# Kernel tuning notes

Hardware: AMD Instinct MI355X
Metric: run time of the kernel (lower is better)

Reference implementation:

```python
import jax, jax.numpy as jnp
import numpy as np

N, E = 50000, 400000
DIN, DH, H, DOUT = 128, 32, 10, 32
HID = H * DH
NEG = 0.2          # LeakyReLU slope in GATv2
EPS_BN = 1e-5

def setup_inputs():
    key = jax.random.key(0)
    ks = jax.random.split(key, 10)
    g = lambda k, shape, fan: jax.random.normal(k, shape, jnp.float32) * (1.0 / np.sqrt(fan))
    return {
        "x": jax.random.normal(ks[0], (N, DIN), jnp.float32),
        "edge_index": jax.random.randint(ks[1], (2, E), 0, N),
        "Wl1": g(ks[2], (DIN, HID), DIN), "bl1": jnp.zeros((HID,), jnp.float32),
        "Wr1": g(ks[3], (DIN, HID), DIN), "br1": jnp.zeros((HID,), jnp.float32),
        "att1": g(ks[4], (H, DH), DH),   "bias1": jnp.zeros((HID,), jnp.float32),
        "gamma": jnp.ones((HID,), jnp.float32), "beta": jnp.zeros((HID,), jnp.float32),
        "prelu_a": jnp.asarray(0.25, jnp.float32),
        "Wl2": g(ks[5], (HID, DOUT), HID), "bl2": jnp.zeros((DOUT,), jnp.float32),
        "Wr2": g(ks[6], (HID, DOUT), HID), "br2": jnp.zeros((DOUT,), jnp.float32),
        "att2": g(ks[7], (1, DOUT), DOUT), "bias2": jnp.zeros((DOUT,), jnp.float32),
    }

def gatv2_layer(x, src, dst, Wl, bl, Wr, br, att, bias, heads, ch, concat):
    n = x.shape[0]
    xl = (x @ Wl + bl).reshape(n, heads, ch)   # source-side (message) transform
    xr = (x @ Wr + br).reshape(n, heads, ch)   # target-side transform
    e = jax.nn.leaky_relu(xl[src] + xr[dst], NEG)          # [E,H,C]
    score = jnp.einsum('ehc,hc->eh', e, att)               # [E,H]
    m = jax.ops.segment_max(score, dst, num_segments=n)    # segment softmax (stable)
    a = jnp.exp(score - m[dst])
    denom = jax.ops.segment_sum(a, dst, num_segments=n)
    alpha = a / (denom[dst] + 1e-16)                       # [E,H]
    out = jax.ops.segment_sum(xl[src] * alpha[:, :, None], dst, num_segments=n)  # [N,H,C]
    out = out.reshape(n, heads * ch) if concat else out.mean(axis=1)
    return out + bias

def reference(x, edge_index, Wl1, bl1, Wr1, br1, att1, bias1, gamma, beta, prelu_a, Wl2, bl2, Wr2, br2, att2, bias2):
    src, dst = edge_index[0], edge_index[1]
    h = gatv2_layer(x, src, dst, Wl1, bl1, Wr1, br1, att1, bias1, H, DH, True)
    mu = h.mean(axis=0)
    var = h.var(axis=0)                                    # BatchNorm1d, batch stats
    h = (h - mu) * jax.lax.rsqrt(var + EPS_BN) * gamma + beta
    h = jnp.where(h >= 0, h, prelu_a * h)                  # PReLU (single shared a)
    out = gatv2_layer(h, src, dst, Wl2, bl2, Wr2, br2, att2, bias2, 1, DOUT, False)
    return out, jax.nn.log_softmax(out, axis=1)
```

## Files before the change

### kernel.cpp

```cpp
#include <hip/hip_runtime.h>
#include <hip/hip_bf16.h>

#define NN 50000
#define NE 400000
#define DIN 128
#define DH 32
#define NH 10
#define HID 320
#define DOUT 32
#define NEG_SLOPE 0.2f
#define EPS_BN 1e-5f

typedef __attribute__((ext_vector_type(8))) short short8;
typedef __attribute__((ext_vector_type(4))) float f32x4;

__device__ inline unsigned short f2bf(float f) {
    unsigned int u = __float_as_uint(f);
    u += 0x7fffu + ((u >> 16) & 1u);
    return (unsigned short)(u >> 16);
}
__device__ inline float bf2f(unsigned short u) {
    return __uint_as_float(((unsigned int)u) << 16);
}
__device__ inline float bflo(unsigned int u) {
    return __uint_as_float(u << 16);
}
__device__ inline float bfhi(unsigned int u) {
    return __uint_as_float(u & 0xffff0000u);
}
__device__ inline float lrelu(float x) { return fmaxf(x, NEG_SLOPE * x); }

__global__ __launch_bounds__(256) void gemm1_kernel(
    const float* __restrict__ x,
    const float* __restrict__ Wl, const float* __restrict__ bl,
    const float* __restrict__ Wr, const float* __restrict__ br,
    unsigned short* __restrict__ xl1, unsigned short* __restrict__ xr1)
{
    __shared__ short xs[64 * 128];
    __shared__ short wt[2][32 * 152];
    const int tid = threadIdx.x;
    const int c0 = blockIdx.x * 32;
    const int r0 = blockIdx.y * 64;

    for (int ch = tid; ch < 2048; ch += 256) {
        int rr = ch >> 5, c4 = (ch & 31) << 2;
        float4 v = make_float4(0.f, 0.f, 0.f, 0.f);
        if (r0 + rr < NN) v = *(const float4*)(x + (size_t)(r0 + rr) * DIN + c4);
        short4 s;
        s.x = (short)f2bf(v.x); s.y = (short)f2bf(v.y);
        s.z = (short)f2bf(v.z); s.w = (short)f2bf(v.w);
        int u = (rr * 128 + c4) ^ ((rr & 7) << 3);
        *(short4*)&xs[u] = s;
    }
    for (int f = tid; f < 2048; f += 256) {
        int mat = f >> 10, fi = f & 1023;
        int k = fi >> 3, cq = (fi & 7) << 2;
        const float* Wp = mat ? Wr : Wl;
        float4 v = *(const float4*)(Wp + (size_t)k * HID + c0 + cq);
        short* dp = &wt[mat][0];
        dp[(cq + 0) * 152 + k] = (short)f2bf(v.x);
        dp[(cq + 1) * 152 + k] = (short)f2bf(v.y);
        dp[(cq + 2) * 152 + k] = (short)f2bf(v.z);
        dp[(cq + 3) * 152 + k] = (short)f2bf(v.w);
    }
    __syncthreads();

    const int w = tid >> 6, lane = tid & 63;
    const int arow = w * 16 + (lane & 15);
    const int kgrp = (lane >> 4) << 3;
    f32x4 acc00 = {}, acc01 = {}, acc10 = {}, acc11 = {};
    #pragma unroll
    for (int kk = 0; kk < 4; ++kk) {
        int au = (arow * 128 + kk * 32 + kgrp) ^ ((arow & 7) << 3);
        short8 a = *(short8*)&xs[au];
        int bu0 = (lane & 15) * 152 + kk * 32 + kgrp;
        int bu1 = (16 + (lane & 15)) * 152 + kk * 32 + kgrp;
        short8 bL0 = *(short8*)&wt[0][bu0];
        short8 bL1 = *(short8*)&wt[0][bu1];
        short8 bR0 = *(short8*)&wt[1][bu0];
        short8 bR1 = *(short8*)&wt[1][bu1];
        acc00 = __builtin_amdgcn_mfma_f32_16x16x32_bf16(a, bL0, acc00, 0, 0, 0);
        acc01 = __builtin_amdgcn_mfma_f32_16x16x32_bf16(a, bL1, acc01, 0, 0, 0);
        acc10 = __builtin_amdgcn_mfma_f32_16x16x32_bf16(a, bR0, acc10, 0, 0, 0);
        acc11 = __builtin_amdgcn_mfma_f32_16x16x32_bf16(a, bR1, acc11, 0, 0, 0);
    }
    const int orow = r0 + w * 16 + ((lane >> 4) << 2);
    #pragma unroll
    for (int cf = 0; cf < 2; ++cf) {
        const int col = c0 + cf * 16 + (lane & 15);
        const float blv = bl[col], brv = br[col];
        const f32x4 aL = cf ? acc01 : acc00;
        const f32x4 aR = cf ? acc11 : acc10;
        #pragma unroll
        for (int reg = 0; reg < 4; ++reg) {
            int row = orow + reg;
            if (row < NN) {
                xl1[(size_t)row * HID + col] = f2bf(aL[reg] + blv);
                xr1[(size_t)row * HID + col] = f2bf(aR[reg] + brv);
            }
        }
    }
}

__global__ void hist_kernel(const int* __restrict__ dst, int* __restrict__ deg) {
    int e = blockIdx.x * blockDim.x + threadIdx.x;
    if (e < NE) atomicAdd(&deg[dst[e]], 1);
}

__global__ __launch_bounds__(1024) void scan_kernel(const int* __restrict__ deg,
        int* __restrict__ row_ptr, int* __restrict__ cursor) {
    __shared__ int sums[1024];
    const int tid = threadIdx.x;
    const int CH = (NN + 1023) / 1024;
    const int st = tid * CH;
    const int en = min(st + CH, NN);
    int s = 0;
    for (int i = st; i < en; ++i) s += deg[i];
    sums[tid] = s;
    __syncthreads();
    for (int off = 1; off < 1024; off <<= 1) {
        int v = (tid >= off) ? sums[tid - off] : 0;
        __syncthreads();
        sums[tid] += v;
        __syncthreads();
    }
    int run = (tid == 0) ? 0 : sums[tid - 1];
    for (int i = st; i < en; ++i) {
        row_ptr[i] = run; cursor[i] = run; run += deg[i];
    }
    if (tid == 1023) row_ptr[NN] = sums[1023];
}

__global__ void scatter_kernel(const int* __restrict__ src, const int* __restrict__ dst,
        int* __restrict__ cursor, int* __restrict__ sorted_src) {
    int e = blockIdx.x * blockDim.x + threadIdx.x;
    if (e < NE) {
        int d = dst[e];
        int p = atomicAdd(&cursor[d], 1);
        sorted_src[p] = src[e];
    }
}

__global__ __launch_bounds__(320) void agg1_kernel(
    const unsigned short* __restrict__ xl1, const unsigned short* __restrict__ xr1,
    const int* __restrict__ row_ptr, const int* __restrict__ sorted_src,
    const float* __restrict__ att1, const float* __restrict__ bias1,
    unsigned short* __restrict__ h1b)
{
    const int t = threadIdx.x;
    const int nsub = t / 80;
    const int r = t - nsub * 80;
    const int h = r >> 3;
    const int l8 = r & 7;
    const int c0 = h * 32 + l8 * 4;
    const int n = blockIdx.x * 4 + nsub;

    const float4 at = *(const float4*)(att1 + c0);
    const unsigned rbase = (unsigned)n * HID + c0;
    uint2 xr4 = *(const uint2*)(xr1 + rbase);
    const float xr0 = bflo(xr4.x), xr1f = bfhi(xr4.x);
    const float xr2 = bflo(xr4.y), xr3 = bfhi(xr4.y);

    const int rp = row_ptr[n];
    const int deg = row_ptr[n + 1] - rp;
    const int* sp = sorted_src + rp;

    float l = 0.f, ac0 = 0.f, ac1 = 0.f, ac2 = 0.f, ac3 = 0.f;
    int i = 0;
    for (; i + 2 <= deg; i += 2) {
        unsigned offA = (unsigned)sp[i] * HID + c0;
        unsigned offB = (unsigned)sp[i + 1] * HID + c0;
        uint2 ua = *(const uint2*)(xl1 + offA);
        uint2 ub = *(const uint2*)(xl1 + offB);
        float xA0 = bflo(ua.x), xA1 = bfhi(ua.x), xA2 = bflo(ua.y), xA3 = bfhi(ua.y);
        float xB0 = bflo(ub.x), xB1 = bfhi(ub.x), xB2 = bflo(ub.y), xB3 = bfhi(ub.y);
        float vA = lrelu(xA0 + xr0) * at.x;
        vA = fmaf(lrelu(xA1 + xr1f), at.y, vA);
        vA = fmaf(lrelu(xA2 + xr2), at.z, vA);
        vA = fmaf(lrelu(xA3 + xr3), at.w, vA);
        float vB = lrelu(xB0 + xr0) * at.x;
        vB = fmaf(lrelu(xB1 + xr1f), at.y, vB);
        vB = fmaf(lrelu(xB2 + xr2), at.z, vB);
        vB = fmaf(lrelu(xB3 + xr3), at.w, vB);
        vA += __shfl_xor(vA, 1); vB += __shfl_xor(vB, 1);
        vA += __shfl_xor(vA, 2); vB += __shfl_xor(vB, 2);
        vA += __shfl_xor(vA, 4); vB += __shfl_xor(vB, 4);
        float pA = __expf(vA), pB = __expf(vB);
        l += pA + pB;
        ac0 = fmaf(pA, xA0, ac0); ac0 = fmaf(pB, xB0, ac0);
        ac1 = fmaf(pA, xA1, ac1); ac1 = fmaf(pB, xB1, ac1);
        ac2 = fmaf(pA, xA2, ac2); ac2 = fmaf(pB, xB2, ac2);
        ac3 = fmaf(pA, xA3, ac3); ac3 = fmaf(pB, xB3, ac3);
    }
    if (i < deg) {
        unsigned offA = (unsigned)sp[i] * HID + c0;
        uint2 ua = *(const uint2*)(xl1 + offA);
        float xA0 = bflo(ua.x), xA1 = bfhi(ua.x), xA2 = bflo(ua.y), xA3 = bfhi(ua.y);
        float vA = lrelu(xA0 + xr0) * at.x;
        vA = fmaf(lrelu(xA1 + xr1f), at.y, vA);
        vA = fmaf(lrelu(xA2 + xr2), at.z, vA);
        vA = fmaf(lrelu(xA3 + xr3), at.w, vA);
        vA += __shfl_xor(vA, 1);
        vA += __shfl_xor(vA, 2);
        vA += __shfl_xor(vA, 4);
        float pA = __expf(vA);
        l += pA;
        ac0 = fmaf(pA, xA0, ac0); ac1 = fmaf(pA, xA1, ac1);
        ac2 = fmaf(pA, xA2, ac2); ac3 = fmaf(pA, xA3, ac3);
    }
    const float inv = 1.f / (l + 1e-16f);
    const float4 bi = *(const float4*)(bias1 + c0);
    uint2 outp;
    outp.x = (unsigned)f2bf(ac0 * inv + bi.x) | ((unsigned)f2bf(ac1 * inv + bi.y) << 16);
    outp.y = (unsigned)f2bf(ac2 * inv + bi.z) | ((unsigned)f2bf(ac3 * inv + bi.w) << 16);
    *(uint2*)(h1b + rbase) = outp;
}

__global__ __launch_bounds__(320) void bnstats_kernel(const unsigned short* __restrict__ h1b,
        double* __restrict__ bn_sum, double* __restrict__ bn_sq) {
    const int tid = threadIdx.x;
    double s = 0.0, q = 0.0;
    for (int n = blockIdx.x; n < NN; n += gridDim.x) {
        float v = bf2f(h1b[(size_t)n * HID + tid]);
        s += v; q += (double)v * v;
    }
    atomicAdd(&bn_sum[tid], s);
    atomicAdd(&bn_sq[tid], q);
}

__global__ void bnfinal_kernel(const double* __restrict__ bn_sum, const double* __restrict__ bn_sq,
        const float* __restrict__ gamma, const float* __restrict__ beta,
        float* __restrict__ scale, float* __restrict__ shift) {
    int c = threadIdx.x;
    double mean = bn_sum[c] / (double)NN;
    double var  = bn_sq[c] / (double)NN - mean * mean;
    float sc = gamma[c] * rsqrtf((float)var + EPS_BN);
    scale[c] = sc;
    shift[c] = beta[c] - (float)mean * sc;
}

__global__ void precast_w2(const float* __restrict__ Wl2, const float* __restrict__ Wr2,
        unsigned short* __restrict__ wl2t, unsigned short* __restrict__ wr2t) {
    int idx = blockIdx.x * 256 + threadIdx.x;
    if (idx < HID * DOUT) {
        int c = idx / HID, k = idx - c * HID;
        wl2t[idx] = f2bf(Wl2[k * DOUT + c]);
        wr2t[idx] = f2bf(Wr2[k * DOUT + c]);
    }
}

__global__ __launch_bounds__(256) void gemm2_kernel(
    const unsigned short* __restrict__ h1b,
    const float* __restrict__ scale, const float* __restrict__ shift,
    const float* __restrict__ prelu_a,
    const unsigned short* __restrict__ wl2t, const unsigned short* __restrict__ wr2t,
    const float* __restrict__ bl2, const float* __restrict__ br2,
    float* __restrict__ xl2, float* __restrict__ xr2)
{
    __shared__ short hs[64 * 320];
    const int tid = threadIdx.x;
    const int r0 = blockIdx.x * 64;
    const float a = prelu_a[0];
    for (int f = tid; f < 5120; f += 256) {
        int e = f << 2;
        int rr = e / 320;
        int cc = e - rr * 320;
        ushort4 hv = make_ushort4(0, 0, 0, 0);
        if (r0 + rr < NN) hv = *(const ushort4*)(h1b + (size_t)(r0 + rr) * HID + cc);
        float4 sc = *(const float4*)(scale + cc);
        float4 sh = *(const float4*)(shift + cc);
        float o0 = bf2f(hv.x) * sc.x + sh.x; o0 = (o0 >= 0.f) ? o0 : a * o0;
        float o1 = bf2f(hv.y) * sc.y + sh.y; o1 = (o1 >= 0.f) ? o1 : a * o1;
        float o2 = bf2f(hv.z) * sc.z + sh.z; o2 = (o2 >= 0.f) ? o2 : a * o2;
        float o3 = bf2f(hv.w) * sc.w + sh.w; o3 = (o3 >= 0.f) ? o3 : a * o3;
        short4 s;
        s.x = (short)f2bf(o0); s.y = (short)f2bf(o1);
        s.z = (short)f2bf(o2); s.w = (short)f2bf(o3);
        int u = (rr * 320 + cc) ^ ((rr & 7) << 3);
        *(short4*)&hs[u] = s;
    }
    __syncthreads();

    const int w = tid >> 6, lane = tid & 63;
    const int arow = w * 16 + (lane & 15);
    const int kgrp = (lane >> 4) << 3;
    const int bcol = lane & 15;
    f32x4 acc00 = {}, acc01 = {}, acc10 = {}, acc11 = {};
    #pragma unroll
    for (int kk = 0; kk < 10; ++kk) {
        int au = (arow * 320 + kk * 32 + kgrp) ^ ((arow & 7) << 3);
        short8 afr = *(short8*)&hs[au];
        const int ko = kk * 32 + kgrp;
        short8 bL0 = *(const short8*)(wl2t + bcol * HID + ko);
        short8 bL1 = *(const short8*)(wl2t + (16 + bcol) * HID + ko);
        short8 bR0 = *(const short8*)(wr2t + bcol * HID + ko);
        short8 bR1 = *(const short8*)(wr2t + (16 + bcol) * HID + ko);
        acc00 = __builtin_amdgcn_mfma_f32_16x16x32_bf16(afr, bL0, acc00, 0, 0, 0);
        acc01 = __builtin_amdgcn_mfma_f32_16x16x32_bf16(afr, bL1, acc01, 0, 0, 0);
        acc10 = __builtin_amdgcn_mfma_f32_16x16x32_bf16(afr, bR0, acc10, 0, 0, 0);
        acc11 = __builtin_amdgcn_mfma_f32_16x16x32_bf16(afr, bR1, acc11, 0, 0, 0);
    }
    const int orow = r0 + w * 16 + ((lane >> 4) << 2);
    #pragma unroll
    for (int cf = 0; cf < 2; ++cf) {
        const int col = cf * 16 + bcol;
        const float blv = bl2[col], brv = br2[col];
        const f32x4 aL = cf ? acc01 : acc00;
        const f32x4 aR = cf ? acc11 : acc10;
        #pragma unroll
        for (int reg = 0; reg < 4; ++reg) {
            int row = orow + reg;
            if (row < NN) {
                xl2[(size_t)row * DOUT + col] = aL[reg] + blv;
                xr2[(size_t)row * DOUT + col] = aR[reg] + brv;
            }
        }
    }
}

__global__ __launch_bounds__(256) void agg2_kernel(
    const float* __restrict__ xl2, const float* __restrict__ xr2,
    const int* __restrict__ row_ptr, const int* __restrict__ sorted_src,
    const float* __restrict__ att2, const float* __restrict__ bias2,
    float* __restrict__ out)
{
    const int t = threadIdx.x;
    const int nsub = t >> 3;
    const int l8 = t & 7;
    const int c0 = l8 * 4;
    const int n = blockIdx.x * 32 + nsub;
    if (n >= NN) return;

    const float4 at = *(const float4*)(att2 + c0);
    const float4 xr4 = *(const float4*)(xr2 + (size_t)n * DOUT + c0);
    const int rp = row_ptr[n];
    const int deg = row_ptr[n + 1] - rp;
    const int* sp = sorted_src + rp;

    float l = 0.f, ac0 = 0.f, ac1 = 0.f, ac2 = 0.f, ac3 = 0.f;
    int i = 0;
    for (; i + 2 <= deg; i += 2) {
        unsigned offA = (unsigned)sp[i] * DOUT + c0;
        unsigned offB = (unsigned)sp[i + 1] * DOUT + c0;
        float4 xa = *(const float4*)(xl2 + offA);
        float4 xb = *(const float4*)(xl2 + offB);
        float vA = lrelu(xa.x + xr4.x) * at.x;
        vA = fmaf(lrelu(xa.y + xr4.y), at.y, vA);
        vA = fmaf(lrelu(xa.z + xr4.z), at.z, vA);
        vA = fmaf(lrelu(xa.w + xr4.w), at.w, vA);
        float vB = lrelu(xb.x + xr4.x) * at.x;
        vB = fmaf(lrelu(xb.y + xr4.y), at.y, vB);
        vB = fmaf(lrelu(xb.z + xr4.z), at.z, vB);
        vB = fmaf(lrelu(xb.w + xr4.w), at.w, vB);
        vA += __shfl_xor(vA, 1); vB += __shfl_xor(vB, 1);
        vA += __shfl_xor(vA, 2); vB += __shfl_xor(vB, 2);
        vA += __shfl_xor(vA, 4); vB += __shfl_xor(vB, 4);
        float pA = __expf(vA), pB = __expf(vB);
        l += pA + pB;
        ac0 = fmaf(pA, xa.x, ac0); ac0 = fmaf(pB, xb.x, ac0);
        ac1 = fmaf(pA, xa.y, ac1); ac1 = fmaf(pB, xb.y, ac1);
        ac2 = fmaf(pA, xa.z, ac2); ac2 = fmaf(pB, xb.z, ac2);
        ac3 = fmaf(pA, xa.w, ac3); ac3 = fmaf(pB, xb.w, ac3);
    }
    if (i < deg) {
        unsigned offA = (unsigned)sp[i] * DOUT + c0;
        float4 xa = *(const float4*)(xl2 + offA);
        float vA = lrelu(xa.x + xr4.x) * at.x;
        vA = fmaf(lrelu(xa.y + xr4.y), at.y, vA);
        vA = fmaf(lrelu(xa.z + xr4.z), at.z, vA);
        vA = fmaf(lrelu(xa.w + xr4.w), at.w, vA);
        vA += __shfl_xor(vA, 1);
        vA += __shfl_xor(vA, 2);
        vA += __shfl_xor(vA, 4);
        float pA = __expf(vA);
        l += pA;
        ac0 = fmaf(pA, xa.x, ac0); ac1 = fmaf(pA, xa.y, ac1);
        ac2 = fmaf(pA, xa.z, ac2); ac3 = fmaf(pA, xa.w, ac3);
    }
    const float inv = 1.f / (l + 1e-16f);
    const float4 bi = *(const float4*)(bias2 + c0);
    float o0 = ac0 * inv + bi.x;
    float o1 = ac1 * inv + bi.y;
    float o2 = ac2 * inv + bi.z;
    float o3 = ac3 * inv + bi.w;
    float mx = fmaxf(fmaxf(o0, o1), fmaxf(o2, o3));
    mx = fmaxf(mx, __shfl_xor(mx, 1));
    mx = fmaxf(mx, __shfl_xor(mx, 2));
    mx = fmaxf(mx, __shfl_xor(mx, 4));
    float se = __expf(o0 - mx) + __expf(o1 - mx) + __expf(o2 - mx) + __expf(o3 - mx);
    se += __shfl_xor(se, 1);
    se += __shfl_xor(se, 2);
    se += __shfl_xor(se, 4);
    float lse = mx + __logf(se);
    float4 ov; ov.x = o0; ov.y = o1; ov.z = o2; ov.w = o3;
    *(float4*)(out + (size_t)n * DOUT + c0) = ov;
    float4 lv; lv.x = o0 - lse; lv.y = o1 - lse; lv.z = o2 - lse; lv.w = o3 - lse;
    *(float4*)(out + (size_t)(NN + n) * DOUT + c0) = lv;
}

extern "C" void kernel_launch(void* const* d_in, const int* in_sizes, int n_in,
                              void* d_out, int out_size, void* d_ws, size_t ws_size,
                              hipStream_t stream)
{
    const float* x       = (const float*)d_in[0];
    const int*   ei      = (const int*)d_in[1];
    const float* Wl1     = (const float*)d_in[2];
    const float* bl1     = (const float*)d_in[3];
    const float* Wr1     = (const float*)d_in[4];
    const float* br1     = (const float*)d_in[5];
    const float* att1    = (const float*)d_in[6];
    const float* bias1   = (const float*)d_in[7];
    const float* gamma   = (const float*)d_in[8];
    const float* beta    = (const float*)d_in[9];
    const float* prelu_a = (const float*)d_in[10];
    const float* Wl2     = (const float*)d_in[11];
    const float* bl2     = (const float*)d_in[12];
    const float* Wr2     = (const float*)d_in[13];
    const float* br2     = (const float*)d_in[14];
    const float* att2    = (const float*)d_in[15];
    const float* bias2   = (const float*)d_in[16];
    const int* src = ei;
    const int* dst = ei + NE;

    char* w = (char*)d_ws;
    unsigned short* xl1b = (unsigned short*)w;
    unsigned short* xr1b = xl1b + (size_t)NN * HID;
    unsigned short* h1b  = xr1b + (size_t)NN * HID;
    char* small = (char*)(h1b + (size_t)NN * HID);
    double* bn_sum = (double*)small;
    double* bn_sq  = bn_sum + HID;
    float* scale   = (float*)(bn_sq + HID);
    float* shift   = scale + HID;
    unsigned short* wl2t = (unsigned short*)(shift + HID);
    unsigned short* wr2t = wl2t + HID * DOUT;
    int* deg       = (int*)(wr2t + HID * DOUT);
    int* cursor    = deg + NN;
    int* sorted    = cursor + NN;
    int* row_ptr   = sorted + NE;
    float* xl2 = (float*)w;
    float* xr2 = (float*)(w + (size_t)NN * DOUT * 4);

    hipMemsetAsync(deg, 0, NN * sizeof(int), stream);
    hipMemsetAsync(bn_sum, 0, 2 * HID * sizeof(double), stream);

    precast_w2<<<(HID * DOUT + 255) / 256, 256, 0, stream>>>(Wl2, Wr2, wl2t, wr2t);
    gemm1_kernel<<<dim3(HID / 32, (NN + 63) / 64), 256, 0, stream>>>(
        x, Wl1, bl1, Wr1, br1, xl1b, xr1b);
    hist_kernel<<<(NE + 255) / 256, 256, 0, stream>>>(dst, deg);
    scan_kernel<<<1, 1024, 0, stream>>>(deg, row_ptr, cursor);
    scatter_kernel<<<(NE + 255) / 256, 256, 0, stream>>>(src, dst, cursor, sorted);
    agg1_kernel<<<NN / 4, 320, 0, stream>>>(xl1b, xr1b, row_ptr, sorted, att1, bias1, h1b);
    bnstats_kernel<<<512, HID, 0, stream>>>(h1b, bn_sum, bn_sq);
    bnfinal_kernel<<<1, HID, 0, stream>>>(bn_sum, bn_sq, gamma, beta, scale, shift);
    gemm2_kernel<<<(NN + 63) / 64, 256, 0, stream>>>(h1b, scale, shift, prelu_a,
        wl2t, wr2t, bl2, br2, xl2, xr2);
    agg2_kernel<<<(NN + 31) / 32, 256, 0, stream>>>(xl2, xr2, row_ptr, sorted, att2, bias2,
        (float*)d_out);
}
```

Baseline: 476.3 us.

## Precast GEMM1 inputs to bf16, remap blocks per XCD, parallelize scan, vectorize BN stats

Adds precast kernels that convert x and the layer-1 weights to bf16 (weights transposed). gemm1 then reads its operands straight from global memory with no LDS staging, and its 1D grid is remapped so that consecutive tiles land on the same XCD. The single-block prefix scan becomes a three-kernel multi-block scan. The BN stats kernel now reads four channels per thread with vector loads. These target the serial scan and the per-block fp32 conversion, at the cost of an extra pass over x and more kernel launches.

```diff
diff --git a/kernel.cpp b/kernel.cpp
--- a/kernel.cpp
+++ b/kernel.cpp
@@ -22,63 +22,71 @@
 __device__ inline float bf2f(unsigned short u) {
     return __uint_as_float(((unsigned int)u) << 16);
 }
-__device__ inline float bflo(unsigned int u) {
-    return __uint_as_float(u << 16);
-}
-__device__ inline float bfhi(unsigned int u) {
-    return __uint_as_float(u & 0xffff0000u);
-}
+__device__ inline float bflo(unsigned int u) { return __uint_as_float(u << 16); }
+__device__ inline float bfhi(unsigned int u) { return __uint_as_float(u & 0xffff0000u); }
 __device__ inline float lrelu(float x) { return fmaxf(x, NEG_SLOPE * x); }
 
+__global__ __launch_bounds__(256) void precast_x(const float* __restrict__ x,
+        unsigned short* __restrict__ xb) {
+    int i = blockIdx.x * 256 + threadIdx.x;
+    if (i < NN * DIN / 4) {
+        float4 v = *(const float4*)(x + (size_t)i * 4);
+        ushort4 s;
+        s.x = f2bf(v.x); s.y = f2bf(v.y); s.z = f2bf(v.z); s.w = f2bf(v.w);
+        *(ushort4*)(xb + (size_t)i * 4) = s;
+    }
+}
+
+__global__ void precast_w1(const float* __restrict__ Wl, const float* __restrict__ Wr,
+        unsigned short* __restrict__ wlt, unsigned short* __restrict__ wrt) {
+    int idx = blockIdx.x * 256 + threadIdx.x;
+    if (idx < HID * DIN) {
+        int c = idx >> 7, k = idx & 127;
+        wlt[idx] = f2bf(Wl[(size_t)k * HID + c]);
+        wrt[idx] = f2bf(Wr[(size_t)k * HID + c]);
+    }
+}
+
+__global__ void precast_w2(const float* __restrict__ Wl2, const float* __restrict__ Wr2,
+        unsigned short* __restrict__ wl2t, unsigned short* __restrict__ wr2t) {
+    int idx = blockIdx.x * 256 + threadIdx.x;
+    if (idx < HID * DOUT) {
+        int c = idx / HID, k = idx - c * HID;
+        wl2t[idx] = f2bf(Wl2[k * DOUT + c]);
+        wr2t[idx] = f2bf(Wr2[k * DOUT + c]);
+    }
+}
+
 __global__ __launch_bounds__(256) void gemm1_kernel(
-    const float* __restrict__ x,
-    const float* __restrict__ Wl, const float* __restrict__ bl,
-    const float* __restrict__ Wr, const float* __restrict__ br,
+    const unsigned short* __restrict__ xb,
+    const unsigned short* __restrict__ wlt, const unsigned short* __restrict__ wrt,
+    const float* __restrict__ bl, const float* __restrict__ br,
     unsigned short* __restrict__ xl1, unsigned short* __restrict__ xr1)
 {
-    __shared__ short xs[64 * 128];
-    __shared__ short wt[2][32 * 152];
-    const int tid = threadIdx.x;
-    const int c0 = blockIdx.x * 32;
-    const int r0 = blockIdx.y * 64;
-
-    for (int ch = tid; ch < 2048; ch += 256) {
-        int rr = ch >> 5, c4 = (ch & 31) << 2;
-        float4 v = make_float4(0.f, 0.f, 0.f, 0.f);
-        if (r0 + rr < NN) v = *(const float4*)(x + (size_t)(r0 + rr) * DIN + c4);
-        short4 s;
-        s.x = (short)f2bf(v.x); s.y = (short)f2bf(v.y);
-        s.z = (short)f2bf(v.z); s.w = (short)f2bf(v.w);
-        int u = (rr * 128 + c4) ^ ((rr & 7) << 3);
-        *(short4*)&xs[u] = s;
-    }
-    for (int f = tid; f < 2048; f += 256) {
-        int mat = f >> 10, fi = f & 1023;
-        int k = fi >> 3, cq = (fi & 7) << 2;
-        const float* Wp = mat ? Wr : Wl;
-        float4 v = *(const float4*)(Wp + (size_t)k * HID + c0 + cq);
-        short* dp = &wt[mat][0];
-        dp[(cq + 0) * 152 + k] = (short)f2bf(v.x);
-        dp[(cq + 1) * 152 + k] = (short)f2bf(v.y);
-        dp[(cq + 2) * 152 + k] = (short)f2bf(v.z);
-        dp[(cq + 3) * 152 + k] = (short)f2bf(v.w);
-    }
-    __syncthreads();
-
-    const int w = tid >> 6, lane = tid & 63;
-    const int arow = w * 16 + (lane & 15);
+    int b = blockIdx.x;
+    int xcd = b & 7, j = b >> 3;
+    int base = (xcd < 4) ? xcd * 978 : 3912 + (xcd - 4) * 977;
+    int t = base + j;
+    int r0 = (t / 10) * 64;
+    int c0 = (t % 10) * 32;
+
+    const int w = threadIdx.x >> 6, lane = threadIdx.x & 63;
+    const int row16 = lane & 15;
     const int kgrp = (lane >> 4) << 3;
+    const int arow = r0 + w * 16 + row16;
+    const int arow_c = min(arow, NN - 1);
+    const unsigned short* ap  = xb  + (size_t)arow_c * DIN + kgrp;
+    const unsigned short* bLp = wlt + (size_t)(c0 + row16) * DIN + kgrp;
+    const unsigned short* bRp = wrt + (size_t)(c0 + row16) * DIN + kgrp;
+
     f32x4 acc00 = {}, acc01 = {}, acc10 = {}, acc11 = {};
     #pragma unroll
     for (int kk = 0; kk < 4; ++kk) {
-        int au = (arow * 128 + kk * 32 + kgrp) ^ ((arow & 7) << 3);
-        short8 a = *(short8*)&xs[au];
-        int bu0 = (lane & 15) * 152 + kk * 32 + kgrp;
-        int bu1 = (16 + (lane & 15)) * 152 + kk * 32 + kgrp;
-        short8 bL0 = *(short8*)&wt[0][bu0];
-        short8 bL1 = *(short8*)&wt[0][bu1];
-        short8 bR0 = *(short8*)&wt[1][bu0];
-        short8 bR1 = *(short8*)&wt[1][bu1];
+        short8 a   = *(const short8*)(ap + kk * 32);
+        short8 bL0 = *(const short8*)(bLp + kk * 32);
+        short8 bL1 = *(const short8*)(bLp + 16 * DIN + kk * 32);
+        short8 bR0 = *(const short8*)(bRp + kk * 32);
+        short8 bR1 = *(const short8*)(bRp + 16 * DIN + kk * 32);
         acc00 = __builtin_amdgcn_mfma_f32_16x16x32_bf16(a, bL0, acc00, 0, 0, 0);
         acc01 = __builtin_amdgcn_mfma_f32_16x16x32_bf16(a, bL1, acc01, 0, 0, 0);
         acc10 = __builtin_amdgcn_mfma_f32_16x16x32_bf16(a, bR0, acc10, 0, 0, 0);
@@ -87,7 +95,7 @@
     const int orow = r0 + w * 16 + ((lane >> 4) << 2);
     #pragma unroll
     for (int cf = 0; cf < 2; ++cf) {
-        const int col = c0 + cf * 16 + (lane & 15);
+        const int col = c0 + cf * 16 + row16;
         const float blv = bl[col], brv = br[col];
         const f32x4 aL = cf ? acc01 : acc00;
         const f32x4 aR = cf ? acc11 : acc10;
@@ -107,28 +115,47 @@
     if (e < NE) atomicAdd(&deg[dst[e]], 1);
 }
 
-__global__ __launch_bounds__(1024) void scan_kernel(const int* __restrict__ deg,
-        int* __restrict__ row_ptr, int* __restrict__ cursor) {
-    __shared__ int sums[1024];
+__global__ __launch_bounds__(1024) void scan1_kernel(const int* __restrict__ deg,
+        int* __restrict__ tmp, int* __restrict__ bsum) {
+    __shared__ int s[1024];
     const int tid = threadIdx.x;
-    const int CH = (NN + 1023) / 1024;
-    const int st = tid * CH;
-    const int en = min(st + CH, NN);
-    int s = 0;
-    for (int i = st; i < en; ++i) s += deg[i];
-    sums[tid] = s;
+    int i = blockIdx.x * 1024 + tid;
+    int v = (i < NN) ? deg[i] : 0;
+    s[tid] = v;
     __syncthreads();
     for (int off = 1; off < 1024; off <<= 1) {
-        int v = (tid >= off) ? sums[tid - off] : 0;
+        int u = (tid >= off) ? s[tid - off] : 0;
         __syncthreads();
-        sums[tid] += v;
+        s[tid] += u;
         __syncthreads();
     }
-    int run = (tid == 0) ? 0 : sums[tid - 1];
-    for (int i = st; i < en; ++i) {
-        row_ptr[i] = run; cursor[i] = run; run += deg[i];
-    }
-    if (tid == 1023) row_ptr[NN] = sums[1023];
+    if (i < NN) tmp[i] = s[tid];
+    if (tid == 1023) bsum[blockIdx.x] = s[1023];
+}
+
+__global__ void scan2_kernel(const int* __restrict__ bsum, int* __restrict__ boff) {
+    int lane = threadIdx.x;
+    int v = (lane < 49) ? bsum[lane] : 0;
+    for (int off = 1; off < 64; off <<= 1) {
+        int u = __shfl_up(v, off);
+        if (lane >= off) v += u;
+    }
+    int excl = __shfl_up(v, 1);
+    if (lane == 0) excl = 0;
+    if (lane < 49) boff[lane] = excl;
+}
+
+__global__ __launch_bounds__(1024) void scan3_kernel(const int* __restrict__ deg,
+        const int* __restrict__ tmp, const int* __restrict__ boff,
+        int* __restrict__ row_ptr, int* __restrict__ cursor) {
+    int i = blockIdx.x * 1024 + threadIdx.x;
+    if (i < NN) {
+        int incl = tmp[i] + boff[blockIdx.x];
+        int st = incl - deg[i];
+        row_ptr[i] = st;
+        cursor[i] = st;
+        if (i == NN - 1) row_ptr[NN] = incl;
+    }
 }
 
 __global__ void scatter_kernel(const int* __restrict__ src, const int* __restrict__ dst,
@@ -219,13 +246,21 @@
 __global__ __launch_bounds__(320) void bnstats_kernel(const unsigned short* __restrict__ h1b,
         double* __restrict__ bn_sum, double* __restrict__ bn_sq) {
     const int tid = threadIdx.x;
-    double s = 0.0, q = 0.0;
-    for (int n = blockIdx.x; n < NN; n += gridDim.x) {
-        float v = bf2f(h1b[(size_t)n * HID + tid]);
-        s += v; q += (double)v * v;
-    }
-    atomicAdd(&bn_sum[tid], s);
-    atomicAdd(&bn_sq[tid], q);
+    const int q = tid / 80;
+    const int c4 = (tid - q * 80) * 4;
+    double s0 = 0, s1 = 0, s2 = 0, s3 = 0, q0 = 0, q1 = 0, q2 = 0, q3 = 0;
+    for (int n = blockIdx.x * 4 + q; n < NN; n += gridDim.x * 4) {
+        uint2 hv = *(const uint2*)(h1b + (size_t)n * HID + c4);
+        float v0 = bflo(hv.x), v1 = bfhi(hv.x), v2 = bflo(hv.y), v3 = bfhi(hv.y);
+        s0 += v0; q0 += (double)v0 * v0;
+        s1 += v1; q1 += (double)v1 * v1;
+        s2 += v2; q2 += (double)v2 * v2;
+        s3 += v3; q3 += (double)v3 * v3;
+    }
+    atomicAdd(&bn_sum[c4 + 0], s0); atomicAdd(&bn_sq[c4 + 0], q0);
+    atomicAdd(&bn_sum[c4 + 1], s1); atomicAdd(&bn_sq[c4 + 1], q1);
+    atomicAdd(&bn_sum[c4 + 2], s2); atomicAdd(&bn_sq[c4 + 2], q2);
+    atomicAdd(&bn_sum[c4 + 3], s3); atomicAdd(&bn_sq[c4 + 3], q3);
 }
 
 __global__ void bnfinal_kernel(const double* __restrict__ bn_sum, const double* __restrict__ bn_sq,
@@ -237,16 +272,6 @@
     float sc = gamma[c] * rsqrtf((float)var + EPS_BN);
     scale[c] = sc;
     shift[c] = beta[c] - (float)mean * sc;
-}
-
-__global__ void precast_w2(const float* __restrict__ Wl2, const float* __restrict__ Wr2,
-        unsigned short* __restrict__ wl2t, unsigned short* __restrict__ wr2t) {
-    int idx = blockIdx.x * 256 + threadIdx.x;
-    if (idx < HID * DOUT) {
-        int c = idx / HID, k = idx - c * HID;
-        wl2t[idx] = f2bf(Wl2[k * DOUT + c]);
-        wr2t[idx] = f2bf(Wr2[k * DOUT + c]);
-    }
 }
 
 __global__ __launch_bounds__(256) void gemm2_kernel(
@@ -426,31 +451,40 @@
     unsigned short* xl1b = (unsigned short*)w;
     unsigned short* xr1b = xl1b + (size_t)NN * HID;
     unsigned short* h1b  = xr1b + (size_t)NN * HID;
-    char* small = (char*)(h1b + (size_t)NN * HID);
-    double* bn_sum = (double*)small;
-    double* bn_sq  = bn_sum + HID;
-    float* scale   = (float*)(bn_sq + HID);
-    float* shift   = scale + HID;
-    unsigned short* wl2t = (unsigned short*)(shift + HID);
-    unsigned short* wr2t = wl2t + HID * DOUT;
-    int* deg       = (int*)(wr2t + HID * DOUT);
-    int* cursor    = deg + NN;
-    int* sorted    = cursor + NN;
-    int* row_ptr   = sorted + NE;
+    char* sm = w + 96000000ull;
+    double* bn_sum = (double*)(sm + 0);
+    double* bn_sq  = (double*)(sm + 2560);
+    float* scale   = (float*)(sm + 5120);
+    float* shift   = (float*)(sm + 6400);
+    unsigned short* wl2t = (unsigned short*)(sm + 7680);
+    unsigned short* wr2t = (unsigned short*)(sm + 28160);
+    unsigned short* wlt1 = (unsigned short*)(sm + 48640);
+    unsigned short* wrt1 = (unsigned short*)(sm + 130560);
+    int* deg     = (int*)(sm + 212480);
+    int* cursor  = (int*)(sm + 412480);
+    int* sorted  = (int*)(sm + 612480);
+    int* row_ptr = (int*)(sm + 2212480);
+    int* tmp     = (int*)(sm + 2412484);
+    int* bsum    = (int*)(sm + 2612484);
+    int* boff    = (int*)(sm + 2612740);
+    unsigned short* xb = (unsigned short*)(sm + 3000000);
     float* xl2 = (float*)w;
     float* xr2 = (float*)(w + (size_t)NN * DOUT * 4);
 
     hipMemsetAsync(deg, 0, NN * sizeof(int), stream);
     hipMemsetAsync(bn_sum, 0, 2 * HID * sizeof(double), stream);
 
+    precast_x<<<(NN * DIN / 4 + 255) / 256, 256, 0, stream>>>(x, xb);
+    precast_w1<<<(HID * DIN + 255) / 256, 256, 0, stream>>>(Wl1, Wr1, wlt1, wrt1);
     precast_w2<<<(HID * DOUT + 255) / 256, 256, 0, stream>>>(Wl2, Wr2, wl2t, wr2t);
-    gemm1_kernel<<<dim3(HID / 32, (NN + 63) / 64), 256, 0, stream>>>(
-        x, Wl1, bl1, Wr1, br1, xl1b, xr1b);
     hist_kernel<<<(NE + 255) / 256, 256, 0, stream>>>(dst, deg);
-    scan_kernel<<<1, 1024, 0, stream>>>(deg, row_ptr, cursor);
+    gemm1_kernel<<<7820, 256, 0, stream>>>(xb, wlt1, wrt1, bl1, br1, xl1b, xr1b);
+    scan1_kernel<<<49, 1024, 0, stream>>>(deg, tmp, bsum);
+    scan2_kernel<<<1, 64, 0, stream>>>(bsum, boff);
+    scan3_kernel<<<49, 1024, 0, stream>>>(deg, tmp, boff, row_ptr, cursor);
     scatter_kernel<<<(NE + 255) / 256, 256, 0, stream>>>(src, dst, cursor, sorted);
     agg1_kernel<<<NN / 4, 320, 0, stream>>>(xl1b, xr1b, row_ptr, sorted, att1, bias1, h1b);
-    bnstats_kernel<<<512, HID, 0, stream>>>(h1b, bn_sum, bn_sq);
+    bnstats_kernel<<<512, 320, 0, stream>>>(h1b, bn_sum, bn_sq);
     bnfinal_kernel<<<1, HID, 0, stream>>>(bn_sum, bn_sq, gamma, beta, scale, shift);
     gemm2_kernel<<<(NN + 63) / 64, 256, 0, stream>>>(h1b, scale, shift, prelu_a,
         wl2t, wr2t, bl2, br2, xl2, xr2);
```

Result: slower. 557.2 us (+17.0%).
